# Kernel optimization log

Hardware: AMD Instinct MI355X
Metric: run time of the kernel (lower is better)

The kernel has to match this reference:

```python
import jax, jax.numpy as jnp
import numpy as np

EPS = 1e-12  # matches torch F.normalize default eps


def setup_inputs() -> dict:
    key = jax.random.key(0)
    k_h, k_s, k_d = jax.random.split(key, 3)
    N, D, E = 100000, 128, 640000
    h = jax.random.normal(k_h, (N, D), dtype=jnp.float32)
    src = jax.random.randint(k_s, (E,), 0, N, dtype=jnp.int64)
    dst = jax.random.randint(k_d, (E,), 0, N, dtype=jnp.int64)
    return {"h": h, "src": src, "dst": dst}


def reference(h, src, dst):
    # L2 normalize node features (F.normalize p=2, dim=-1)
    norm = jnp.linalg.norm(h, axis=-1, keepdims=True)
    norm_h = h / jnp.maximum(norm, EPS)
    # SDDMM: per-edge dot product of normalized src/dst features -> [E, 1]
    cos = jnp.sum(norm_h[src] * norm_h[dst], axis=-1, keepdims=True)
    return cos
```

## Files before the change

### kernel.cpp

```cpp
#include <hip/hip_runtime.h>
#include <math.h>

#define EPS 1e-12f

__device__ inline unsigned short f32_to_bf16_rn(float f) {
    unsigned int u = __float_as_uint(f);
    u += 0x7fffu + ((u >> 16) & 1u);
    return (unsigned short)(u >> 16);
}

__global__ void __launch_bounds__(256) norm_bf16_kernel(const float* __restrict__ h,
                                                        unsigned int* __restrict__ hn,
                                                        int N) {
    int row  = (blockIdx.x * blockDim.x + threadIdx.x) >> 6;
    int lane = threadIdx.x & 63;
    if (row >= N) return;
    const float2* rp = (const float2*)(h + (size_t)row * 128);
    float2 v = rp[lane];
    float s = v.x * v.x + v.y * v.y;
    #pragma unroll
    for (int off = 32; off > 0; off >>= 1)
        s += __shfl_xor(s, off, 64);
    float r = 1.0f / fmaxf(sqrtf(s), EPS);
    unsigned int lo = f32_to_bf16_rn(v.x * r);
    unsigned int hi = f32_to_bf16_rn(v.y * r);
    hn[(size_t)row * 64 + lane] = lo | (hi << 16);
}

__device__ inline float dot2_bf16pair(unsigned int u, unsigned int v) {
    float ul = __uint_as_float(u << 16);
    float uh = __uint_as_float(u & 0xffff0000u);
    float vl = __uint_as_float(v << 16);
    float vh = __uint_as_float(v & 0xffff0000u);
    return fmaf(ul, vl, uh * vh);
}

__device__ inline float dot8_uint4(uint4 a, uint4 b) {
    float p = dot2_bf16pair(a.x, b.x);
    p += dot2_bf16pair(a.y, b.y);
    p += dot2_bf16pair(a.z, b.z);
    p += dot2_bf16pair(a.w, b.w);
    return p;
}

__global__ void __launch_bounds__(256) edge_bf16_kernel4(const uint4* __restrict__ hn,
                                                         const int* __restrict__ src,
                                                         const int* __restrict__ dst,
                                                         float* __restrict__ out,
                                                         int E) {
    int tid = blockIdx.x * blockDim.x + threadIdx.x;
    int e   = tid >> 2;
    int sub = threadIdx.x & 3;
    if (e >= E) return;
    int s = src[e];
    int d = dst[e];
    const uint4* rs = hn + (size_t)s * 16;
    const uint4* rd = hn + (size_t)d * 16;
    uint4 a0 = rs[sub];
    uint4 a1 = rs[sub + 4];
    uint4 a2 = rs[sub + 8];
    uint4 a3 = rs[sub + 12];
    uint4 b0 = rd[sub];
    uint4 b1 = rd[sub + 4];
    uint4 b2 = rd[sub + 8];
    uint4 b3 = rd[sub + 12];
    float p = dot8_uint4(a0, b0);
    p += dot8_uint4(a1, b1);
    p += dot8_uint4(a2, b2);
    p += dot8_uint4(a3, b3);
    p += __shfl_xor(p, 2, 64);
    p += __shfl_xor(p, 1, 64);
    if (sub == 0)
        out[e] = p;
}

__global__ void __launch_bounds__(256) rnorm_kernel(const float* __restrict__ h,
                                                    float* __restrict__ rnorm,
                                                    int N) {
    int row  = (blockIdx.x * blockDim.x + threadIdx.x) >> 6;
    int lane = threadIdx.x & 63;
    if (row >= N) return;
    const float2* rp = (const float2*)(h + (size_t)row * 128);
    float2 v = rp[lane];
    float s = v.x * v.x + v.y * v.y;
    #pragma unroll
    for (int off = 32; off > 0; off >>= 1)
        s += __shfl_xor(s, off, 64);
    if (lane == 0)
        rnorm[row] = 1.0f / fmaxf(sqrtf(s), EPS);
}

__global__ void __launch_bounds__(256) edge_f32_kernel(const float* __restrict__ h,
                                                       const int* __restrict__ src,
                                                       const int* __restrict__ dst,
                                                       const float* __restrict__ rnorm,
                                                       float* __restrict__ out,
                                                       int E) {
    int tid = blockIdx.x * blockDim.x + threadIdx.x;
    int e   = tid >> 5;
    int sub = threadIdx.x & 31;
    if (e >= E) return;
    int s = src[e];
    int d = dst[e];
    const float4* rs = (const float4*)(h + (size_t)s * 128);
    const float4* rd = (const float4*)(h + (size_t)d * 128);
    float4 a = rs[sub];
    float4 b = rd[sub];
    float p = a.x * b.x + a.y * b.y + a.z * b.z + a.w * b.w;
    #pragma unroll
    for (int off = 16; off > 0; off >>= 1)
        p += __shfl_xor(p, off, 64);
    if (sub == 0)
        out[e] = p * rnorm[s] * rnorm[d];
}

extern "C" void kernel_launch(void* const* d_in, const int* in_sizes, int n_in,
                              void* d_out, int out_size, void* d_ws, size_t ws_size,
                              hipStream_t stream) {
    const float* h   = (const float*)d_in[0];
    const int*   src = (const int*)d_in[1];
    const int*   dst = (const int*)d_in[2];
    float*       out = (float*)d_out;

    const int N = in_sizes[0] / 128;
    const int E = in_sizes[1];

    size_t hn_bytes = (size_t)N * 128 * 2;

    if (ws_size >= hn_bytes) {
        unsigned int* hn = (unsigned int*)d_ws;
        {
            int grid = (N * 64 + 255) / 256;
            norm_bf16_kernel<<<grid, 256, 0, stream>>>(h, hn, N);
        }
        {
            long long threads = (long long)E * 4;
            int grid = (int)((threads + 255) / 256);
            edge_bf16_kernel4<<<grid, 256, 0, stream>>>((const uint4*)hn, src, dst, out, E);
        }
    } else {
        float* rnorm = (float*)d_ws;
        {
            int grid = (N * 64 + 255) / 256;
            rnorm_kernel<<<grid, 256, 0, stream>>>(h, rnorm, N);
        }
        {
            int grid = (E * 32 + 255) / 256;
            edge_f32_kernel<<<grid, 256, 0, stream>>>(h, src, dst, rnorm, out, E);
        }
    }
}
```

Measured before the change: 136.0 us.

## Quantize normalized features to int8 with per-row scale and use sdot4

The normalize pass now stores each row as symmetric int8 with a per-row float scale that folds in the L2 norm. The edge kernel reads 128-byte rows instead of 256-byte bf16 rows and accumulates the dot product with packed int8 dot instructions. This halves the gather traffic that dominates the edge pass. In exchange it adds two scale loads per edge and loses accuracy compared with bf16, which may break the tolerance check.

Result: faster. 111.3 us (-18.2%).

```diff
diff --git a/kernel.cpp b/kernel.cpp
--- a/kernel.cpp
+++ b/kernel.cpp
@@ -3,75 +3,85 @@
 
 #define EPS 1e-12f
 
-__device__ inline unsigned short f32_to_bf16_rn(float f) {
-    unsigned int u = __float_as_uint(f);
-    u += 0x7fffu + ((u >> 16) & 1u);
-    return (unsigned short)(u >> 16);
+__global__ void __launch_bounds__(256) norm_q8_kernel(const float* __restrict__ h,
+                                                      unsigned int* __restrict__ hq,
+                                                      float* __restrict__ scale,
+                                                      int N) {
+    int tid  = blockIdx.x * blockDim.x + threadIdx.x;
+    int row  = tid >> 5;
+    int lane = threadIdx.x & 31;
+    if (row >= N) return;
+    const float4* rp = (const float4*)(h + (size_t)row * 128);
+    float4 v = rp[lane];
+    float ss = v.x * v.x + v.y * v.y + v.z * v.z + v.w * v.w;
+    float ma = fmaxf(fmaxf(fabsf(v.x), fabsf(v.y)), fmaxf(fabsf(v.z), fabsf(v.w)));
+    #pragma unroll
+    for (int off = 16; off > 0; off >>= 1) {
+        ss += __shfl_xor(ss, off, 64);
+        ma = fmaxf(ma, __shfl_xor(ma, off, 64));
+    }
+    float r  = 1.0f / fmaxf(sqrtf(ss), EPS);
+    float qs = 127.0f / fmaxf(ma, 1e-30f);
+    int qx = __float2int_rn(v.x * qs);
+    int qy = __float2int_rn(v.y * qs);
+    int qz = __float2int_rn(v.z * qs);
+    int qw = __float2int_rn(v.w * qs);
+    unsigned int pack = ((unsigned int)qx & 0xffu)
+                      | (((unsigned int)qy & 0xffu) << 8)
+                      | (((unsigned int)qz & 0xffu) << 16)
+                      | (((unsigned int)qw & 0xffu) << 24);
+    hq[(size_t)row * 32 + lane] = pack;
+    if (lane == 0)
+        scale[row] = ma * r * (1.0f / 127.0f);
 }
 
-__global__ void __launch_bounds__(256) norm_bf16_kernel(const float* __restrict__ h,
-                                                        unsigned int* __restrict__ hn,
-                                                        int N) {
-    int row  = (blockIdx.x * blockDim.x + threadIdx.x) >> 6;
-    int lane = threadIdx.x & 63;
-    if (row >= N) return;
-    const float2* rp = (const float2*)(h + (size_t)row * 128);
-    float2 v = rp[lane];
-    float s = v.x * v.x + v.y * v.y;
-    #pragma unroll
-    for (int off = 32; off > 0; off >>= 1)
-        s += __shfl_xor(s, off, 64);
-    float r = 1.0f / fmaxf(sqrtf(s), EPS);
-    unsigned int lo = f32_to_bf16_rn(v.x * r);
-    unsigned int hi = f32_to_bf16_rn(v.y * r);
-    hn[(size_t)row * 64 + lane] = lo | (hi << 16);
+__device__ inline int dot4i8(unsigned int a, unsigned int b, int c) {
+#if __has_builtin(__builtin_amdgcn_sdot4)
+    return __builtin_amdgcn_sdot4((int)a, (int)b, c, false);
+#else
+    c += (int)(signed char)(a)       * (int)(signed char)(b);
+    c += (int)(signed char)(a >> 8)  * (int)(signed char)(b >> 8);
+    c += (int)(signed char)(a >> 16) * (int)(signed char)(b >> 16);
+    c += (int)(signed char)(a >> 24) * (int)(signed char)(b >> 24);
+    return c;
+#endif
 }
 
-__device__ inline float dot2_bf16pair(unsigned int u, unsigned int v) {
-    float ul = __uint_as_float(u << 16);
-    float uh = __uint_as_float(u & 0xffff0000u);
-    float vl = __uint_as_float(v << 16);
-    float vh = __uint_as_float(v & 0xffff0000u);
-    return fmaf(ul, vl, uh * vh);
+__device__ inline int dot16(uint4 a, uint4 b, int c) {
+    c = dot4i8(a.x, b.x, c);
+    c = dot4i8(a.y, b.y, c);
+    c = dot4i8(a.z, b.z, c);
+    c = dot4i8(a.w, b.w, c);
+    return c;
 }
 
-__device__ inline float dot8_uint4(uint4 a, uint4 b) {
-    float p = dot2_bf16pair(a.x, b.x);
-    p += dot2_bf16pair(a.y, b.y);
-    p += dot2_bf16pair(a.z, b.z);
-    p += dot2_bf16pair(a.w, b.w);
-    return p;
-}
-
-__global__ void __launch_bounds__(256) edge_bf16_kernel4(const uint4* __restrict__ hn,
-                                                         const int* __restrict__ src,
-                                                         const int* __restrict__ dst,
-                                                         float* __restrict__ out,
-                                                         int E) {
+__global__ void __launch_bounds__(256) edge_q8_kernel(const uint4* __restrict__ hq,
+                                                      const int* __restrict__ src,
+                                                      const int* __restrict__ dst,
+                                                      const float* __restrict__ scale,
+                                                      float* __restrict__ out,
+                                                      int E) {
     int tid = blockIdx.x * blockDim.x + threadIdx.x;
     int e   = tid >> 2;
     int sub = threadIdx.x & 3;
     if (e >= E) return;
     int s = src[e];
     int d = dst[e];
-    const uint4* rs = hn + (size_t)s * 16;
-    const uint4* rd = hn + (size_t)d * 16;
+    const uint4* rs = hq + (size_t)s * 8;
+    const uint4* rd = hq + (size_t)d * 8;
     uint4 a0 = rs[sub];
     uint4 a1 = rs[sub + 4];
-    uint4 a2 = rs[sub + 8];
-    uint4 a3 = rs[sub + 12];
     uint4 b0 = rd[sub];
     uint4 b1 = rd[sub + 4];
-    uint4 b2 = rd[sub + 8];
-    uint4 b3 = rd[sub + 12];
-    float p = dot8_uint4(a0, b0);
-    p += dot8_uint4(a1, b1);
-    p += dot8_uint4(a2, b2);
-    p += dot8_uint4(a3, b3);
-    p += __shfl_xor(p, 2, 64);
-    p += __shfl_xor(p, 1, 64);
+    float sa = scale[s];
+    float sd = scale[d];
+    int acc = 0;
+    acc = dot16(a0, b0, acc);
+    acc = dot16(a1, b1, acc);
+    acc += __shfl_xor(acc, 2, 64);
+    acc += __shfl_xor(acc, 1, 64);
     if (sub == 0)
-        out[e] = p;
+        out[e] = (float)acc * sa * sd;
 }
 
 __global__ void __launch_bounds__(256) rnorm_kernel(const float* __restrict__ h,
@@ -125,18 +135,22 @@
     const int N = in_sizes[0] / 128;
     const int E = in_sizes[1];
 
-    size_t hn_bytes = (size_t)N * 128 * 2;
+    size_t hq_bytes    = (size_t)N * 128;
+    size_t scale_bytes = (size_t)N * sizeof(float);
 
-    if (ws_size >= hn_bytes) {
-        unsigned int* hn = (unsigned int*)d_ws;
+    if (ws_size >= hq_bytes + scale_bytes) {
+        unsigned int* hq    = (unsigned int*)d_ws;
+        float*        scale = (float*)((char*)d_ws + hq_bytes);
         {
-            int grid = (N * 64 + 255) / 256;
-            norm_bf16_kernel<<<grid, 256, 0, stream>>>(h, hn, N);
+            long long threads = (long long)N * 32;
+            int grid = (int)((threads + 255) / 256);
+            norm_q8_kernel<<<grid, 256, 0, stream>>>(h, hq, scale, N);
         }
         {
             long long threads = (long long)E * 4;
             int grid = (int)((threads + 255) / 256);
-            edge_bf16_kernel4<<<grid, 256, 0, stream>>>((const uint4*)hn, src, dst, out, E);
+            edge_q8_kernel<<<grid, 256, 0, stream>>>((const uint4*)hq, src, dst,
+                                                     scale, out, E);
         }
     } else {
         float* rnorm = (float*)d_ws;
```
